# Kernel optimization log

Measured on AMD Instinct MI355X. Metric: run time of the kernel, lower is better.

Reference implementation:

```python
import jax, jax.numpy as jnp
import numpy as np

V, H = 32000, 1024  # vocab / hidden, must match init_kwargs


def setup_inputs() -> dict:
    key = jax.random.key(0)
    ks = jax.random.split(key, 10)
    L, B, S = 32, 64, 16
    s = 1.0 / np.sqrt(H)
    emb_w = jax.random.normal(ks[0], (V, H), jnp.float32)
    emb_w = emb_w.at[0].set(0.0)  # padding_idx=0 row is zero
    return {
        "target_tensor": jax.random.randint(ks[1], (L, B), 0, V),
        "encoder_outputs": jax.random.normal(ks[2], (S, B, H), jnp.float32),
        "hidden": jax.random.normal(ks[3], (1, B, H), jnp.float32),
        "emb_w": emb_w,
        "w_ih": jax.random.uniform(ks[4], (3 * H, H), jnp.float32, -s, s),
        "w_hh": jax.random.uniform(ks[5], (3 * H, H), jnp.float32, -s, s),
        "b_ih": jax.random.uniform(ks[6], (3 * H,), jnp.float32, -s, s),
        "b_hh": jax.random.uniform(ks[7], (3 * H,), jnp.float32, -s, s),
        "fc_w": jax.random.uniform(ks[8], (V, H), jnp.float32, -s, s),
        "fc_b": jax.random.uniform(ks[9], (V,), jnp.float32, -s, s),
    }


def _gru_cell(x, h, w_ih, w_hh, b_ih, b_hh):
    # PyTorch GRU cell. x, h: [B, H]
    gi = x @ w_ih.T + b_ih            # [B, 3H]
    gh = h @ w_hh.T + b_hh            # [B, 3H]
    i_r, i_z, i_n = jnp.split(gi, 3, axis=-1)
    h_r, h_z, h_n = jnp.split(gh, 3, axis=-1)
    r = jax.nn.sigmoid(i_r + h_r)
    z = jax.nn.sigmoid(i_z + h_z)
    n = jnp.tanh(i_n + r * h_n)
    return (1.0 - z) * n + z * h


def reference(target_tensor, encoder_outputs, hidden, emb_w, w_ih, w_hh, b_ih, b_hh, fc_w, fc_b):
    L, B = target_tensor.shape
    # teacher forcing: step 0 uses all-ones token, step i uses target[i-1]
    ones0 = jnp.ones((1, B), dtype=target_tensor.dtype)
    inputs = jnp.concatenate([ones0, target_tensor[:-1]], axis=0)  # [L, B]
    h0 = hidden[0]  # [B, H]

    def step(h, idx):
        x = jax.nn.relu(emb_w[idx])            # [B, H] (dropout in eval mode)
        h_new = _gru_cell(x, h, w_ih, w_hh, b_ih, b_hh)
        return h_new, h_new

    h_last, outs = jax.lax.scan(step, h0, inputs)  # outs: [L, B, H]
    logits = jnp.einsum("lbh,vh->lbv", outs, fc_w) + fc_b  # [L, B, V]
    log_probs = jax.nn.log_softmax(logits, axis=-1)
    return log_probs, h_last[None]  # hidden: [1, B, H]
```

## Files before the change

### kernel.cpp

```cpp
#include <hip/hip_runtime.h>

typedef float  f32x4 __attribute__((ext_vector_type(4)));
typedef short  s16x8 __attribute__((ext_vector_type(8)));

#define AS1 __attribute__((address_space(1)))
#define AS3 __attribute__((address_space(3)))

__device__ __forceinline__ void gload_lds16(const void* g, void* l) {
  __builtin_amdgcn_global_load_lds((AS1 void*)(g), (AS3 void*)(l), 16, 0, 0);
}

__device__ __forceinline__ void mfma_bf16(f32x4& d, s16x8 a, s16x8 b) {
  asm volatile("v_mfma_f32_16x16x32_bf16 %0, %1, %2, %0" : "+v"(d) : "v"(a), "v"(b));
}

__device__ __forceinline__ void gload_b128(s16x8& d, const void* p) {
  asm volatile("global_load_dwordx4 %0, %1, off" : "=v"(d) : "v"(p));
}
__device__ __forceinline__ void gload_f128(f32x4& d, const void* p) {
  asm volatile("global_load_dwordx4 %0, %1, off" : "=v"(d) : "v"(p));
}

__device__ __forceinline__ unsigned short f2bf(float f) {
  union { float f; unsigned u; } v; v.f = f;
  unsigned u = v.u;
  unsigned r = u + 0x7fffu + ((u >> 16) & 1u);
  return (unsigned short)(r >> 16);
}
__device__ __forceinline__ float bf2f(unsigned short u) {
  union { unsigned u; float f; } v; v.u = ((unsigned)u) << 16; return v.f;
}

__launch_bounds__(256)
__global__ void cvt_bf16(const float* __restrict__ in, unsigned short* __restrict__ out, int n4) {
  for (int i = blockIdx.x * blockDim.x + threadIdx.x; i < n4; i += gridDim.x * blockDim.x) {
    float4 v = ((const float4*)in)[i];
    ushort4 u;
    u.x = f2bf(v.x); u.y = f2bf(v.y); u.z = f2bf(v.z); u.w = f2bf(v.w);
    ((ushort4*)out)[i] = u;
  }
}

__launch_bounds__(256)
__global__ void init_h(const float* __restrict__ hid, float* __restrict__ hA,
                       unsigned short* __restrict__ hbf) {
  int i = blockIdx.x * 256 + threadIdx.x;
  float4 v = ((const float4*)hid)[i];
  ((float4*)hA)[i] = v;
  ushort4 u; u.x = f2bf(v.x); u.y = f2bf(v.y); u.z = f2bf(v.z); u.w = f2bf(v.w);
  ((ushort4*)hbf)[i] = u;
}

__launch_bounds__(256)
__global__ void embed_relu(const int* __restrict__ tgt, const float* __restrict__ emb,
                           unsigned short* __restrict__ xbf) {
  int bid = blockIdx.x;
  int t = bid >> 6, b = bid & 63;
  int tok = (t == 0) ? 1 : tgt[(t - 1) * 64 + b];
  int c = threadIdx.x;
  float4 v = ((const float4*)(emb + (size_t)tok * 1024))[c];
  v.x = fmaxf(v.x, 0.f); v.y = fmaxf(v.y, 0.f); v.z = fmaxf(v.z, 0.f); v.w = fmaxf(v.w, 0.f);
  ushort4 u; u.x = f2bf(v.x); u.y = f2bf(v.y); u.z = f2bf(v.z); u.w = f2bf(v.w);
  ((ushort4*)(xbf + (size_t)bid * 1024))[c] = u;
}

template<bool STATS, bool OUTBF>
__launch_bounds__(256)
__global__ void gemm_bt(const unsigned short* __restrict__ A,
                        const unsigned short* __restrict__ B,
                        const float* __restrict__ bias,
                        float* __restrict__ Cf,
                        unsigned short* __restrict__ Cb,
                        float2* __restrict__ stats,
                        int N, int K, int mTiles, int nTilesTotal) {
  __shared__ unsigned short As[128 * 64];
  __shared__ unsigned short Bs[128 * 64];
  __shared__ float2 sstat[2][128];

  const int tid = threadIdx.x;
  int bid = blockIdx.x;
  {
    int q = gridDim.x >> 3;
    bid = (bid & 7) * q + (bid >> 3);
  }
  const int tileN = bid / mTiles;
  const int tileM = bid % mTiles;
  const int m0 = tileM * 128, n0 = tileN * 128;
  const int lane = tid & 63;
  const int w = tid >> 6, wr = w >> 1, wc = w & 1;
  const int lr = lane & 15, lg = lane >> 4;

  f32x4 acc[4][4];
#pragma unroll
  for (int m = 0; m < 4; ++m)
#pragma unroll
    for (int n = 0; n < 4; ++n) acc[m][n] = (f32x4){0.f, 0.f, 0.f, 0.f};

  const int crow = tid >> 3;
  const int cj   = tid & 7;

  for (int kt = 0; kt < K; kt += 64) {
#pragma unroll
    for (int it = 0; it < 4; ++it) {
      int row = it * 32 + crow;
      int sb = ((cj * 16) ^ ((row & 7) << 4)) >> 1;
      gload_lds16(A + (size_t)(m0 + row) * K + kt + sb, &As[row * 64 + cj * 8]);
      gload_lds16(B + (size_t)(n0 + row) * K + kt + sb, &Bs[row * 64 + cj * 8]);
    }
    __syncthreads();
#pragma unroll
    for (int kk = 0; kk < 2; ++kk) {
      s16x8 af[4], bfr[4];
#pragma unroll
      for (int m = 0; m < 4; ++m) {
        int row = wr * 64 + m * 16 + lr;
        int off = ((kk * 64 + lg * 16) ^ ((row & 7) << 4)) >> 1;
        af[m] = *reinterpret_cast<const s16x8*>(&As[row * 64 + off]);
      }
#pragma unroll
      for (int n = 0; n < 4; ++n) {
        int row = wc * 64 + n * 16 + lr;
        int off = ((kk * 64 + lg * 16) ^ ((row & 7) << 4)) >> 1;
        bfr[n] = *reinterpret_cast<const s16x8*>(&Bs[row * 64 + off]);
      }
#pragma unroll
      for (int m = 0; m < 4; ++m)
#pragma unroll
        for (int n = 0; n < 4; ++n) mfma_bf16(acc[m][n], af[m], bfr[n]);
    }
    __syncthreads();
  }

  float bv[4];
#pragma unroll
  for (int n = 0; n < 4; ++n) bv[n] = bias[n0 + wc * 64 + n * 16 + lr];
#pragma unroll
  for (int m = 0; m < 4; ++m)
#pragma unroll
    for (int n = 0; n < 4; ++n)
#pragma unroll
      for (int j = 0; j < 4; ++j) acc[m][n][j] += bv[n];

#pragma unroll
  for (int m = 0; m < 4; ++m) {
    int rbase = m0 + wr * 64 + m * 16 + lg * 4;
#pragma unroll
    for (int j = 0; j < 4; ++j) {
      size_t roff = (size_t)(rbase + j) * N;
#pragma unroll
      for (int n = 0; n < 4; ++n) {
        size_t idx = roff + n0 + wc * 64 + n * 16 + lr;
        if (OUTBF) Cb[idx] = f2bf(acc[m][n][j]);
        else       Cf[idx] = acc[m][n][j];
      }
    }
  }

  if (STATS) {
#pragma unroll
    for (int m = 0; m < 4; ++m) {
#pragma unroll
      for (int j = 0; j < 4; ++j) {
        float vmax = acc[m][0][j];
#pragma unroll
        for (int n = 1; n < 4; ++n) vmax = fmaxf(vmax, acc[m][n][j]);
#pragma unroll
        for (int s = 1; s < 16; s <<= 1) vmax = fmaxf(vmax, __shfl_xor(vmax, s, 64));
        float ss = 0.f;
#pragma unroll
        for (int n = 0; n < 4; ++n) ss += __expf(acc[m][n][j] - vmax);
#pragma unroll
        for (int s = 1; s < 16; s <<= 1) ss += __shfl_xor(ss, s, 64);
        if (lr == 0) sstat[wc][wr * 64 + m * 16 + lg * 4 + j] = make_float2(vmax, ss);
      }
    }
    __syncthreads();
    if (tid < 128) {
      float2 a = sstat[0][tid], b = sstat[1][tid];
      float Mx = fmaxf(a.x, b.x);
      float S = a.y * __expf(a.x - Mx) + b.y * __expf(b.x - Mx);
      stats[(size_t)(m0 + tid) * nTilesTotal + tileN] = make_float2(Mx, S);
    }
  }
}

template<bool OUTBF>
__launch_bounds__(256, 1)
__global__ void scan_fused(const unsigned short* __restrict__ whh,
                           const float* __restrict__ gi,
                           const float* __restrict__ bhh,
                           float* __restrict__ h,
                           unsigned short* __restrict__ outs_bf,
                           unsigned* __restrict__ bar,
                           const unsigned short* __restrict__ fcw,
                           const float* __restrict__ fcb,
                           float* __restrict__ Cf,
                           unsigned short* __restrict__ Cb,
                           float2* __restrict__ stats) {
  __shared__ char smem[96 * 1024];
  const int tid = threadIdx.x, lane = tid & 63, w = tid >> 6;
  const int lr = lane & 15, lg = lane >> 4;
  const int bid = blockIdx.x;

  if (bid < 64) {
    char* lds = smem;
    const int j0 = bid * 16;

    for (int c = tid; c < 6144; c += 256) {
      int chunk = c >> 6, u = c & 63;
      int g = chunk >> 5, K = chunk & 31;
      gload_lds16(whh + (size_t)(g * 1024 + j0 + (u & 15)) * 1024 + K * 32 + (u >> 4) * 8,
                  lds + (size_t)c * 16);
    }

    const int b  = w * 16 + lr;
    const int c0 = j0 + lg * 4;

    float4 bhr = *(const float4*)(bhh + c0);
    float4 bhz = *(const float4*)(bhh + 1024 + c0);
    float4 bhn = *(const float4*)(bhh + 2048 + c0);

    float4 hv = *(const float4*)(h + (size_t)b * 1024 + c0);
    f32x4 cr, cz, cn;
    {
      const float* g0 = gi + (size_t)b * 3072 + c0;
      cr = *(const f32x4*)(g0);
      cz = *(const f32x4*)(g0 + 1024);
      cn = *(const f32x4*)(g0 + 2048);
    }

    __syncthreads();

#define WAITV(n)                                               \
  asm volatile("s_waitcnt vmcnt(" #n ")" ::: "memory");        \
  __builtin_amdgcn_sched_barrier(0);
#define ISSUE8(q, ibase)                                       \
  _Pragma("unroll")                                            \
  for (int j = 0; j < 8; ++j)                                  \
    gload_b128(q[j], rowp + ((ibase) + j) * 4 + lg);
#define MFMA8(q, ibase)                                        \
  _Pragma("unroll")                                            \
  for (int j = 0; j < 8; ++j) {                                \
    _Pragma("unroll")                                          \
    for (int g = 0; g < 3; ++g) {                              \
      s16x8 wf = *reinterpret_cast<const s16x8*>(              \
          lds + (size_t)(g * 32 + (ibase) + j) * 1024 + lane * 16); \
      mfma_bf16(acc[g], wf, q[j]);                             \
    }                                                          \
  }

    for (int t = 0; t < 32; ++t) {
      const s16x8* rowp = (const s16x8*)(outs_bf + (size_t)t * 65536 + (size_t)b * 1024);

      f32x4 nr, nz, nn;
      {
        int tn = (t < 31) ? t + 1 : 31;
        const float* gn = gi + ((size_t)tn * 64 + b) * 3072 + c0;
        gload_f128(nr, gn);
        gload_f128(nz, gn + 1024);
        gload_f128(nn, gn + 2048);
      }
      s16x8 qa[8], qb[8];
      ISSUE8(qa, 0)
      ISSUE8(qb, 8)

      f32x4 acc[3];
#pragma unroll
      for (int g = 0; g < 3; ++g) acc[g] = (f32x4){0.f, 0.f, 0.f, 0.f};

      WAITV(8)
      MFMA8(qa, 0)
      ISSUE8(qa, 16)
      WAITV(8)
      MFMA8(qb, 8)
      ISSUE8(qb, 24)
      WAITV(8)
      MFMA8(qa, 16)
      WAITV(0)
      MFMA8(qb, 24)

      float hvv[4] = {hv.x, hv.y, hv.z, hv.w};
      float crr[4] = {cr[0], cr[1], cr[2], cr[3]}, czz[4] = {cz[0], cz[1], cz[2], cz[3]},
            cnn[4] = {cn[0], cn[1], cn[2], cn[3]};
      float brr[4] = {bhr.x, bhr.y, bhr.z, bhr.w}, bzz[4] = {bhz.x, bhz.y, bhz.z, bhz.w},
            bnn[4] = {bhn.x, bhn.y, bhn.z, bhn.w};
      unsigned long long pk = 0;
#pragma unroll
      for (int j = 0; j < 4; ++j) {
        float r = 1.f / (1.f + __expf(-(crr[j] + acc[0][j] + brr[j])));
        float z = 1.f / (1.f + __expf(-(czz[j] + acc[1][j] + bzz[j])));
        float n = tanhf(cnn[j] + r * (acc[2][j] + bnn[j]));
        hvv[j] = n + z * (hvv[j] - n);
        pk |= (unsigned long long)f2bf(hvv[j]) << (16 * j);
      }
      hv = (float4){hvv[0], hvv[1], hvv[2], hvv[3]};
      cr = nr; cz = nz; cn = nn;

      __hip_atomic_store(
          (unsigned long long*)(outs_bf + (size_t)(t + 1) * 65536 + (size_t)b * 1024 + c0),
          pk, __ATOMIC_RELAXED, __HIP_MEMORY_SCOPE_AGENT);

      asm volatile("s_waitcnt vmcnt(0)" ::: "memory");
      __syncthreads();
      if (tid == 0)
        __hip_atomic_store(&bar[bid * 32], (unsigned)(t + 1),
                           __ATOMIC_RELAXED, __HIP_MEMORY_SCOPE_AGENT);
      if (t < 31) {
        if (tid < 64) {
          while (__hip_atomic_load(&bar[tid * 32], __ATOMIC_RELAXED,
                                   __HIP_MEMORY_SCOPE_AGENT) < (unsigned)(t + 1))
            __builtin_amdgcn_s_sleep(1);
        }
        __syncthreads();
      }
    }
#undef WAITV
#undef ISSUE8
#undef MFMA8

    *(float4*)(h + (size_t)b * 1024 + c0) = hv;

  } else {
    unsigned short* As0 = (unsigned short*)smem;
    unsigned short* Bs0 = (unsigned short*)(smem + 16384);
    unsigned short* As1 = (unsigned short*)(smem + 32768);
    unsigned short* Bs1 = (unsigned short*)(smem + 49152);
    float2* sstat = (float2*)(smem + 65536);

    const unsigned short* Ag = outs_bf + 65536;
    const unsigned short* Bg = fcw;
    const int cb = bid - 64;
    const int wr = w >> 1, wc = w & 1;
    const int crow = tid >> 3, cj = tid & 7;

#define CSTAGE(Asp, Bsp, kt)                                                        \
    _Pragma("unroll")                                                               \
    for (int it = 0; it < 4; ++it) {                                                \
      int row = it * 32 + crow;                                                     \
      int sb = ((cj * 16) ^ ((row & 7) << 4)) >> 1;                                 \
      gload_lds16(Ag + (size_t)(m0 + row) * 1024 + (kt) + sb, Asp + row * 64 + cj * 8); \
      gload_lds16(Bg + (size_t)(n0 + row) * 1024 + (kt) + sb, Bsp + row * 64 + cj * 8); \
    }
#define CCOMP(Asp, Bsp)                                                             \
    _Pragma("unroll")                                                               \
    for (int kk = 0; kk < 2; ++kk) {                                                \
      s16x8 af[4], bfr[4];                                                          \
      _Pragma("unroll")                                                             \
      for (int m = 0; m < 4; ++m) {                                                 \
        int row = wr * 64 + m * 16 + lr;                                            \
        int off = ((kk * 64 + lg * 16) ^ ((row & 7) << 4)) >> 1;                    \
        af[m] = *reinterpret_cast<const s16x8*>(&Asp[row * 64 + off]);              \
      }                                                                             \
      _Pragma("unroll")                                                             \
      for (int n = 0; n < 4; ++n) {                                                 \
        int row = wc * 64 + n * 16 + lr;                                            \
        int off = ((kk * 64 + lg * 16) ^ ((row & 7) << 4)) >> 1;                    \
        bfr[n] = *reinterpret_cast<const s16x8*>(&Bsp[row * 64 + off]);             \
      }                                                                             \
      _Pragma("unroll")                                                             \
      for (int m = 0; m < 4; ++m)                                                   \
        _Pragma("unroll")                                                           \
        for (int n = 0; n < 4; ++n) mfma_bf16(acc[m][n], af[m], bfr[n]);            \
    }

    for (int tau = cb; tau < 4000; tau += 176) {
      int mt = tau / 250, nt = tau - mt * 250;
      int m0 = mt * 128, n0 = nt * 128;

      unsigned need = 2u * (unsigned)mt + 2u;
      while (!__all(__hip_atomic_load(&bar[lane * 32], __ATOMIC_RELAXED,
                                      __HIP_MEMORY_SCOPE_AGENT) >= need))
        __builtin_amdgcn_s_sleep(2);

      f32x4 acc[4][4];
#pragma unroll
      for (int m = 0; m < 4; ++m)
#pragma unroll
        for (int n = 0; n < 4; ++n) acc[m][n] = (f32x4){0.f, 0.f, 0.f, 0.f};

      CSTAGE(As0, Bs0, 0)
      __syncthreads();
#pragma unroll 2
      for (int ki = 0; ki < 16; ++ki) {
        if (ki & 1) {
          if (ki < 15) CSTAGE(As0, Bs0, (ki + 1) * 64)
          CCOMP(As1, Bs1)
        } else {
          if (ki < 15) CSTAGE(As1, Bs1, (ki + 1) * 64)
          CCOMP(As0, Bs0)
        }
        __syncthreads();
      }

      float bv[4];
#pragma unroll
      for (int n = 0; n < 4; ++n) bv[n] = fcb[n0 + wc * 64 + n * 16 + lr];
#pragma unroll
      for (int m = 0; m < 4; ++m)
#pragma unroll
        for (int n = 0; n < 4; ++n)
#pragma unroll
          for (int j = 0; j < 4; ++j) acc[m][n][j] += bv[n];

#pragma unroll
      for (int m = 0; m < 4; ++m) {
        int rbase = m0 + wr * 64 + m * 16 + lg * 4;
#pragma unroll
        for (int j = 0; j < 4; ++j) {
          size_t roff = (size_t)(rbase + j) * 32000;
#pragma unroll
          for (int n = 0; n < 4; ++n) {
            size_t idx = roff + n0 + wc * 64 + n * 16 + lr;
            if (OUTBF) Cb[idx] = f2bf(acc[m][n][j]);
            else       Cf[idx] = acc[m][n][j];
          }
        }
      }

#pragma unroll
      for (int m = 0; m < 4; ++m) {
#pragma unroll
        for (int j = 0; j < 4; ++j) {
          float vmax = acc[m][0][j];
#pragma unroll
          for (int n = 1; n < 4; ++n) vmax = fmaxf(vmax, acc[m][n][j]);
#pragma unroll
          for (int s = 1; s < 16; s <<= 1) vmax = fmaxf(vmax, __shfl_xor(vmax, s, 64));
          float ss = 0.f;
#pragma unroll
          for (int n = 0; n < 4; ++n) ss += __expf(acc[m][n][j] - vmax);
#pragma unroll
          for (int s = 1; s < 16; s <<= 1) ss += __shfl_xor(ss, s, 64);
          if (lr == 0) sstat[wc * 128 + wr * 64 + m * 16 + lg * 4 + j] = make_float2(vmax, ss);
        }
      }
      __syncthreads();
      if (tid < 128) {
        float2 a = sstat[tid], b2 = sstat[128 + tid];
        float Mx = fmaxf(a.x, b2.x);
        float S = a.y * __expf(a.x - Mx) + b2.y * __expf(b2.x - Mx);
        stats[(size_t)(m0 + tid) * 250 + nt] = make_float2(Mx, S);
      }
      __syncthreads();
    }
#undef CSTAGE
#undef CCOMP
  }
}

__launch_bounds__(256)
__global__ void reduce_logz(const float2* __restrict__ stats, float* __restrict__ logZ, int nt) {
  int gid = blockIdx.x * blockDim.x + threadIdx.x;
  int row = gid >> 6, lane = gid & 63;
  const float2* s = stats + (size_t)row * nt;
  float M = -3.4e38f;
  for (int i = lane; i < nt; i += 64) M = fmaxf(M, s[i].x);
#pragma unroll
  for (int sh = 1; sh < 64; sh <<= 1) M = fmaxf(M, __shfl_xor(M, sh, 64));
  float S = 0.f;
  for (int i = lane; i < nt; i += 64) S += s[i].y * __expf(s[i].x - M);
#pragma unroll
  for (int sh = 1; sh < 64; sh <<= 1) S += __shfl_xor(S, sh, 64);
  if (lane == 0) logZ[row] = M + logf(S);
}

__launch_bounds__(256)
__global__ void fixup_bf(const unsigned short* __restrict__ lbf, const float* __restrict__ logZ,
                         float* __restrict__ out) {
  const int n8 = 2048 * 32000 / 8;
  for (int i = blockIdx.x * 256 + threadIdx.x; i < n8; i += gridDim.x * 256) {
    s16x8 v = reinterpret_cast<const s16x8*>(lbf)[i];
    float z = logZ[i / 4000];
    float4 o0, o1;
    o0.x = bf2f((unsigned short)v[0]) - z; o0.y = bf2f((unsigned short)v[1]) - z;
    o0.z = bf2f((unsigned short)v[2]) - z; o0.w = bf2f((unsigned short)v[3]) - z;
    o1.x = bf2f((unsigned short)v[4]) - z; o1.y = bf2f((unsigned short)v[5]) - z;
    o1.z = bf2f((unsigned short)v[6]) - z; o1.w = bf2f((unsigned short)v[7]) - z;
    reinterpret_cast<float4*>(out)[2 * i]     = o0;
    reinterpret_cast<float4*>(out)[2 * i + 1] = o1;
  }
}

__launch_bounds__(256)
__global__ void fixup_rmw(float* __restrict__ out, const float* __restrict__ logZ) {
  const size_t total4 = 65536000u / 4u;
  for (size_t i = blockIdx.x * (size_t)blockDim.x + threadIdx.x; i < total4;
       i += (size_t)gridDim.x * blockDim.x) {
    float4 v = ((float4*)out)[i];
    int row = (int)((i * 4) / 32000);
    float z = logZ[row];
    v.x -= z; v.y -= z; v.z -= z; v.w -= z;
    ((float4*)out)[i] = v;
  }
}

__launch_bounds__(256)
__global__ void copy_h(const float* __restrict__ src, float* __restrict__ dst) {
  int i = blockIdx.x * 256 + threadIdx.x;
  ((float4*)dst)[i] = ((const float4*)src)[i];
}

extern "C" void kernel_launch(void* const* d_in, const int* in_sizes, int n_in,
                              void* d_out, int out_size, void* d_ws, size_t ws_size,
                              hipStream_t stream) {
  const int*   target = (const int*)d_in[0];
  const float* hidden = (const float*)d_in[2];
  const float* emb    = (const float*)d_in[3];
  const float* wih    = (const float*)d_in[4];
  const float* whh    = (const float*)d_in[5];
  const float* bih    = (const float*)d_in[6];
  const float* bhh    = (const float*)d_in[7];
  const float* fcw    = (const float*)d_in[8];
  const float* fcb    = (const float*)d_in[9];
  float* out = (float*)d_out;

  const int L = 32, B = 64, H = 1024, V = 32000;
  const int LB = L * B;
  const int NT_LOGITS = V / 128;
  const int MT = LB / 128;

  char* ws = (char*)d_ws;
  size_t off = 0;
  auto alloc = [&](size_t bytes) -> void* {
    void* p = ws + off;
    off += (bytes + 255) & ~(size_t)255;
    return p;
  };
  unsigned short* wih_bf  = (unsigned short*)alloc((size_t)3 * H * H * 2);
  unsigned short* whh_bf  = (unsigned short*)alloc((size_t)3 * H * H * 2);
  unsigned short* fcw_bf  = (unsigned short*)alloc((size_t)V * H * 2);
  unsigned short* x_bf    = (unsigned short*)alloc((size_t)LB * H * 2);
  unsigned short* outs_bf = (unsigned short*)alloc((size_t)(L + 1) * B * H * 2);
  float*          gi      = (float*)alloc((size_t)LB * 3 * H * 4);
  float*          hA      = (float*)alloc((size_t)B * H * 4);
  float2*         stats   = (float2*)alloc((size_t)LB * NT_LOGITS * 8);
  float*          logZ    = (float*)alloc((size_t)LB * 4);
  unsigned*       bar     = (unsigned*)alloc(64 * 128);
  size_t lbf_bytes = (size_t)LB * V * 2;
  unsigned short* lbf = (unsigned short*)(ws + off);
  bool big = (off + lbf_bytes) <= ws_size;
  (void)in_sizes; (void)n_in; (void)out_size;

  cvt_bf16<<<2048, 256, 0, stream>>>(wih, wih_bf, 3 * H * H / 4);
  cvt_bf16<<<2048, 256, 0, stream>>>(whh, whh_bf, 3 * H * H / 4);
  cvt_bf16<<<2048, 256, 0, stream>>>(fcw, fcw_bf, V * H / 4);

  init_h<<<64, 256, 0, stream>>>(hidden, hA, outs_bf);

  embed_relu<<<LB, 256, 0, stream>>>(target, emb, x_bf);

  gemm_bt<false, false><<<(3 * H / 128) * MT, 256, 0, stream>>>(
      x_bf, wih_bf, bih, gi, nullptr, nullptr, 3 * H, H, MT, 3 * H / 128);

  hipMemsetAsync(bar, 0, 64 * 128, stream);
  if (big) {
    scan_fused<true><<<240, 256, 0, stream>>>(
        whh_bf, gi, bhh, hA, outs_bf, bar, fcw_bf, fcb, nullptr, lbf, stats);
    reduce_logz<<<LB * 64 / 256, 256, 0, stream>>>(stats, logZ, NT_LOGITS);
    fixup_bf<<<2048, 256, 0, stream>>>(lbf, logZ, out);
  } else {
    scan_fused<false><<<240, 256, 0, stream>>>(
        whh_bf, gi, bhh, hA, outs_bf, bar, fcw_bf, fcb, out, nullptr, stats);
    reduce_logz<<<LB * 64 / 256, 256, 0, stream>>>(stats, logZ, NT_LOGITS);
    fixup_rmw<<<2048, 256, 0, stream>>>(out, logZ);
  }

  copy_h<<<64, 256, 0, stream>>>(hA, out + (size_t)LB * V);
}
```

Baseline: 581.7 us.

## Triple-buffer FC GEMM LDS staging with explicit vmcnt waits and barriers

Replaces the double-buffered LDS pipeline in the vocab-projection GEMM blocks with a three-stage ring that prefetches two K-tiles ahead. It uses explicit s_waitcnt vmcnt counts and raw s_barrier with sched_barrier in place of __syncthreads, and fully unrolls the K loop. The dependency spin-wait on the recurrent-step barrier now runs only in wave 0 with a longer sleep, and the other waves wait at a block barrier. The goal is to hide global-to-LDS load latency and cut polling traffic, at the cost of more LDS (96KB, which may reduce occupancy) and hand-tuned wait counts that must match the number of issued loads.

```diff
diff --git a/kernel.cpp b/kernel.cpp
--- a/kernel.cpp
+++ b/kernel.cpp
@@ -321,46 +321,46 @@
     *(float4*)(h + (size_t)b * 1024 + c0) = hv;
 
   } else {
-    unsigned short* As0 = (unsigned short*)smem;
-    unsigned short* Bs0 = (unsigned short*)(smem + 16384);
-    unsigned short* As1 = (unsigned short*)(smem + 32768);
-    unsigned short* Bs1 = (unsigned short*)(smem + 49152);
-    float2* sstat = (float2*)(smem + 65536);
-
     const unsigned short* Ag = outs_bf + 65536;
     const unsigned short* Bg = fcw;
     const int cb = bid - 64;
     const int wr = w >> 1, wc = w & 1;
     const int crow = tid >> 3, cj = tid & 7;
 
-#define CSTAGE(Asp, Bsp, kt)                                                        \
-    _Pragma("unroll")                                                               \
-    for (int it = 0; it < 4; ++it) {                                                \
-      int row = it * 32 + crow;                                                     \
-      int sb = ((cj * 16) ^ ((row & 7) << 4)) >> 1;                                 \
-      gload_lds16(Ag + (size_t)(m0 + row) * 1024 + (kt) + sb, Asp + row * 64 + cj * 8); \
-      gload_lds16(Bg + (size_t)(n0 + row) * 1024 + (kt) + sb, Bsp + row * 64 + cj * 8); \
-    }
-#define CCOMP(Asp, Bsp)                                                             \
-    _Pragma("unroll")                                                               \
-    for (int kk = 0; kk < 2; ++kk) {                                                \
-      s16x8 af[4], bfr[4];                                                          \
-      _Pragma("unroll")                                                             \
-      for (int m = 0; m < 4; ++m) {                                                 \
-        int row = wr * 64 + m * 16 + lr;                                            \
-        int off = ((kk * 64 + lg * 16) ^ ((row & 7) << 4)) >> 1;                    \
-        af[m] = *reinterpret_cast<const s16x8*>(&Asp[row * 64 + off]);              \
-      }                                                                             \
-      _Pragma("unroll")                                                             \
-      for (int n = 0; n < 4; ++n) {                                                 \
-        int row = wc * 64 + n * 16 + lr;                                            \
-        int off = ((kk * 64 + lg * 16) ^ ((row & 7) << 4)) >> 1;                    \
-        bfr[n] = *reinterpret_cast<const s16x8*>(&Bsp[row * 64 + off]);             \
-      }                                                                             \
-      _Pragma("unroll")                                                             \
-      for (int m = 0; m < 4; ++m)                                                   \
-        _Pragma("unroll")                                                           \
-        for (int n = 0; n < 4; ++n) mfma_bf16(acc[m][n], af[m], bfr[n]);            \
+#define CWAIT(n)                                               \
+    asm volatile("s_waitcnt vmcnt(" #n ")" ::: "memory");      \
+    __builtin_amdgcn_sched_barrier(0);
+#define CBAR()                                                 \
+    __builtin_amdgcn_s_barrier();                              \
+    __builtin_amdgcn_sched_barrier(0);
+#define CSTG(base, kt)                                                                   \
+    _Pragma("unroll")                                                                    \
+    for (int it = 0; it < 4; ++it) {                                                     \
+      int row = it * 32 + crow;                                                          \
+      int sb = ((cj * 16) ^ ((row & 7) << 4)) >> 1;                                      \
+      gload_lds16(Ag + (size_t)(m0 + row) * 1024 + (kt) + sb, (base) + row * 128 + cj * 16);         \
+      gload_lds16(Bg + (size_t)(n0 + row) * 1024 + (kt) + sb, (base) + 16384 + row * 128 + cj * 16); \
+    }
+#define CCMP(base)                                                                       \
+    _Pragma("unroll")                                                                    \
+    for (int kk = 0; kk < 2; ++kk) {                                                     \
+      s16x8 af[4], bfr[4];                                                               \
+      _Pragma("unroll")                                                                  \
+      for (int m = 0; m < 4; ++m) {                                                      \
+        int row = wr * 64 + m * 16 + lr;                                                 \
+        int off = (kk * 64 + lg * 16) ^ ((row & 7) << 4);                                \
+        af[m] = *reinterpret_cast<const s16x8*>((base) + row * 128 + off);               \
+      }                                                                                  \
+      _Pragma("unroll")                                                                  \
+      for (int n = 0; n < 4; ++n) {                                                      \
+        int row = wc * 64 + n * 16 + lr;                                                 \
+        int off = (kk * 64 + lg * 16) ^ ((row & 7) << 4);                                \
+        bfr[n] = *reinterpret_cast<const s16x8*>((base) + 16384 + row * 128 + off);      \
+      }                                                                                  \
+      _Pragma("unroll")                                                                  \
+      for (int m = 0; m < 4; ++m)                                                        \
+        _Pragma("unroll")                                                                \
+        for (int n = 0; n < 4; ++n) mfma_bf16(acc[m][n], af[m], bfr[n]);                 \
     }
 
     for (int tau = cb; tau < 4000; tau += 176) {
@@ -368,9 +368,12 @@
       int m0 = mt * 128, n0 = nt * 128;
 
       unsigned need = 2u * (unsigned)mt + 2u;
-      while (!__all(__hip_atomic_load(&bar[lane * 32], __ATOMIC_RELAXED,
-                                      __HIP_MEMORY_SCOPE_AGENT) >= need))
-        __builtin_amdgcn_s_sleep(2);
+      if (w == 0) {
+        while (!__all(__hip_atomic_load(&bar[lane * 32], __ATOMIC_RELAXED,
+                                        __HIP_MEMORY_SCOPE_AGENT) >= need))
+          __builtin_amdgcn_s_sleep(32);
+      }
+      CBAR()
 
       f32x4 acc[4][4];
 #pragma unroll
@@ -378,18 +381,22 @@
 #pragma unroll
         for (int n = 0; n < 4; ++n) acc[m][n] = (f32x4){0.f, 0.f, 0.f, 0.f};
 
-      CSTAGE(As0, Bs0, 0)
-      __syncthreads();
-#pragma unroll 2
+      CSTG(smem, 0)
+      CSTG(smem + 32768, 64)
+
+#pragma unroll
       for (int ki = 0; ki < 16; ++ki) {
-        if (ki & 1) {
-          if (ki < 15) CSTAGE(As0, Bs0, (ki + 1) * 64)
-          CCOMP(As1, Bs1)
-        } else {
-          if (ki < 15) CSTAGE(As1, Bs1, (ki + 1) * 64)
-          CCOMP(As0, Bs0)
+        char* cur = smem + (ki % 3) * 32768;
+        if (ki + 2 < 16) {
+          char* nxt = smem + ((ki + 2) % 3) * 32768;
+          CSTG(nxt, (ki + 2) * 64)
         }
-        __syncthreads();
+        if (ki < 14)       { CWAIT(16) }
+        else if (ki == 14) { CWAIT(8) }
+        else               { CWAIT(0) }
+        CBAR()
+        CCMP(cur)
+        CBAR()
       }
 
       float bv[4];
@@ -417,6 +424,7 @@
         }
       }
 
+      float2* sstat = (float2*)smem;
 #pragma unroll
       for (int m = 0; m < 4; ++m) {
 #pragma unroll
@@ -443,8 +451,10 @@
       }
       __syncthreads();
     }
-#undef CSTAGE
-#undef CCOMP
+#undef CWAIT
+#undef CBAR
+#undef CSTG
+#undef CCMP
   }
 }
 
```

After: 552.5 us. -5.0%, faster.
